# Kernel tuning notes

Hardware: AMD Instinct MI355X
Metric: run time of the kernel (lower is better)

The kernel has to match this reference:

```python
import jax, jax.numpy as jnp
import numpy as np

B, N, D = 4, 8192, 512
L, W, S = 64, 64, 32  # num_tokens, win_size, stride


def setup_inputs() -> dict:
    key = jax.random.key(0)
    ks = jax.random.split(key, 12)
    inp = {
        "feats": jax.random.normal(ks[0], (B, N, D), jnp.float32),
        "coords": jax.random.normal(ks[1], (B, N, 2), jnp.float32) * 100.0,
        "mask": jnp.zeros((B, N), dtype=bool),
        "z": jax.random.normal(ks[2], (L, D), jnp.float32) * 0.02,
        "Wq": jax.random.normal(ks[3], (D, D), jnp.float32) * 0.01,
        "Wk": jax.random.normal(ks[4], (D, D), jnp.float32) * 0.01,
        "Wv": jax.random.normal(ks[5], (D, D), jnp.float32) * 0.01,
        "W1": jax.random.normal(ks[6], (D, 2), jnp.float32) * 0.05,
        "b1": jnp.zeros((D,), jnp.float32),
        "W2": jax.random.normal(ks[7], (D, D), jnp.float32) * 0.01,
        "b2": jnp.zeros((D,), jnp.float32),
        "Wo": jax.random.normal(ks[8], (D, D), jnp.float32) * 0.01,
        "bo": jnp.zeros((D,), jnp.float32),
    }
    return inp


def reference(feats, coords, mask, z, Wq, Wk, Wv, W1, b1, W2, b2, Wo, bo):
    # mask is all-False: every token valid, N_valid == N, segments are
    # contiguous blocks of P = N // L tokens (seg_id = floor(i*L/N)).
    Bz, Nn, Dd = feats.shape
    Ll = z.shape[0]
    P = Nn // Ll  # tokens per segment

    # LayerNorm over feature dim (no affine, eps=1e-5 as in F.layer_norm)
    mu = feats.mean(-1, keepdims=True)
    var = feats.var(-1, keepdims=True)
    f_ln = (feats - mu) * jax.lax.rsqrt(var + 1e-5)

    # per-sample coordinate normalization (torch std is unbiased, ddof=1)
    c_mu = coords.mean(1, keepdims=True)
    c_sd = coords.std(1, keepdims=True, ddof=1) + 1e-8
    c_n = (coords - c_mu) / c_sd

    f_seg = f_ln.reshape(Bz, Ll, P, Dd)
    c_seg = c_n.reshape(Bz, Ll, P, 2)

    # static sliding windows within each segment (last window may be partial)
    starts = np.arange(0, P, S)                      # [nw]
    idx = starts[:, None] + np.arange(W)[None, :]    # [nw, W]
    valid = jnp.asarray(idx < P)                     # [nw, W] bool
    idx_c = np.minimum(idx, P - 1)
    cnt = valid.sum(-1).astype(feats.dtype)          # [nw]

    f_win = f_seg[:, :, idx_c]                       # [B,L,nw,W,D]
    c_win = c_seg[:, :, idx_c]                       # [B,L,nw,W,2]

    vmask = valid.astype(feats.dtype)[None, None, :, :, None]
    c_mean = (c_win * vmask).sum(3) / cnt[None, None, :, None]   # [B,L,nw,2]
    pos_in = c_win - c_mean[:, :, :, None, :]
    h = jax.nn.relu(jnp.einsum('blnwc,dc->blnwd', pos_in, W1) + b1)
    pos_bias = jnp.einsum('blnwd,ed->blnwe', h, W2) + b2

    q = z @ Wq.T                                     # [L,D]
    k = jnp.einsum('blnwd,ed->blnwe', f_win, Wk) + pos_bias
    v = jnp.einsum('blnwd,ed->blnwe', f_win, Wv)

    temperature = jnp.sqrt(jnp.asarray(Dd, feats.dtype))
    logits = jnp.einsum('ld,blnwd->blnw', q, k) / temperature
    logits = jnp.clip(logits, -10.0, 10.0)
    logits = jnp.where(valid[None, None], logits, -jnp.inf)
    attn = jax.nn.softmax(logits, axis=-1)           # [B,L,nw,W]

    z_win = jnp.einsum('blnw,blnwd->blnd', attn, v)  # [B,L,nw,D]
    z_l = z_win.mean(2)                              # average over windows
    return z_l @ Wo.T + bo                           # [B,L,D]
```

## Files before the change

### kernel.cpp

```cpp
#include <hip/hip_runtime.h>

#define Bz 4
#define Nn 8192
#define Dd 512
#define Ll 64
#define Pp 128
#define Ww 64
#define Ss 32
#define NW 4

__global__ __launch_bounds__(256) void pre1(
    const float* __restrict__ coords, const float* __restrict__ b2,
    const float* __restrict__ Wq, const float* __restrict__ Wk,
    const float* __restrict__ W2,
    const float* __restrict__ Wv, const float* __restrict__ Wo,
    float* __restrict__ cstats,
    float* __restrict__ M1, float* __restrict__ M2,
    float* __restrict__ WvoT, float* __restrict__ vb8) {
    __shared__ float As[64][68];
    __shared__ float Bs[64][68];
    __shared__ float b2s[64];
    __shared__ double dred[16];
    int bid = blockIdx.x, tid = threadIdx.x;
    int wv = tid >> 6, lane = tid & 63;

    if (bid < 192) {
        int role = bid >> 6;
        int wb = bid & 63;
        int m0 = (wb >> 3) * 64;
        int n0 = (wb & 7) * 64;
        const float* Amat = (role == 2) ? Wv : Wq;
        const float* Bmat = (role == 0) ? Wk : (role == 1) ? W2 : Wo;
        float* Cmat = (role == 0) ? M1 : (role == 1) ? M2 : WvoT;
        int tx = tid & 15, ty = tid >> 4;
        float4 acc[4];
#pragma unroll
        for (int i = 0; i < 4; ++i) acc[i] = make_float4(0.f, 0.f, 0.f, 0.f);

        for (int k0 = 0; k0 < Dd; k0 += 64) {
            {
                int kk = tid >> 4, q4 = (tid & 15) * 4;
#pragma unroll
                for (int i = 0; i < 4; ++i) {
                    int k = kk + 16 * i;
                    *(float4*)&As[k][q4] =
                        *(const float4*)&Amat[(size_t)(k0 + k) * Dd + m0 + q4];
                }
                if (role != 2) {
#pragma unroll
                    for (int i = 0; i < 4; ++i) {
                        int k = kk + 16 * i;
                        *(float4*)&Bs[k][q4] =
                            *(const float4*)&Bmat[(size_t)(k0 + k) * Dd + n0 + q4];
                    }
                } else {
                    int d = tid >> 2;
#pragma unroll
                    for (int j = 0; j < 4; ++j) {
                        int c0 = (tid & 3) * 16 + 4 * j;
                        float4 v = *(const float4*)&Bmat[(size_t)(n0 + d) * Dd + k0 + c0];
                        Bs[c0 + 0][d] = v.x; Bs[c0 + 1][d] = v.y;
                        Bs[c0 + 2][d] = v.z; Bs[c0 + 3][d] = v.w;
                    }
                }
            }
            __syncthreads();
#pragma unroll 8
            for (int kk = 0; kk < 64; ++kk) {
                float4 a4 = *(const float4*)&As[kk][ty * 4];
                float4 b4 = *(const float4*)&Bs[kk][tx * 4];
                acc[0].x = fmaf(a4.x, b4.x, acc[0].x); acc[0].y = fmaf(a4.x, b4.y, acc[0].y);
                acc[0].z = fmaf(a4.x, b4.z, acc[0].z); acc[0].w = fmaf(a4.x, b4.w, acc[0].w);
                acc[1].x = fmaf(a4.y, b4.x, acc[1].x); acc[1].y = fmaf(a4.y, b4.y, acc[1].y);
                acc[1].z = fmaf(a4.y, b4.z, acc[1].z); acc[1].w = fmaf(a4.y, b4.w, acc[1].w);
                acc[2].x = fmaf(a4.z, b4.x, acc[2].x); acc[2].y = fmaf(a4.z, b4.y, acc[2].y);
                acc[2].z = fmaf(a4.z, b4.z, acc[2].z); acc[2].w = fmaf(a4.z, b4.w, acc[2].w);
                acc[3].x = fmaf(a4.w, b4.x, acc[3].x); acc[3].y = fmaf(a4.w, b4.y, acc[3].y);
                acc[3].z = fmaf(a4.w, b4.z, acc[3].z); acc[3].w = fmaf(a4.w, b4.w, acc[3].w);
            }
            __syncthreads();
        }
#pragma unroll
        for (int i = 0; i < 4; ++i)
            *(float4*)&Cmat[(size_t)(m0 + ty * 4 + i) * Dd + n0 + tx * 4] = acc[i];
    } else if (bid < 200) {
        int j = bid - 192;
        if (tid < 64) b2s[tid] = b2[j * 64 + tid];
        __syncthreads();
        float a0 = 0.f, a1 = 0.f;
#pragma unroll 4
        for (int ee = 0; ee < 64; ++ee) {
            int e = j * 64 + ee;
            float be = b2s[ee];
            a0 = fmaf(be, Wq[(size_t)e * Dd + tid], a0);
            a1 = fmaf(be, Wq[(size_t)e * Dd + tid + 256], a1);
        }
        vb8[j * Dd + tid] = a0;
        vb8[j * Dd + tid + 256] = a1;
    } else {
        int b = bid - 200;
        double sx = 0, sy = 0, sxx = 0, syy = 0;
        const float4* cp = (const float4*)(coords + (size_t)b * Nn * 2);
        for (int i = tid; i < Nn / 2; i += 256) {
            float4 v = cp[i];
            sx  += (double)v.x + (double)v.z;
            sy  += (double)v.y + (double)v.w;
            sxx += (double)v.x * v.x + (double)v.z * v.z;
            syy += (double)v.y * v.y + (double)v.w * v.w;
        }
        for (int o = 32; o > 0; o >>= 1) {
            sx  += __shfl_down(sx,  o); sy  += __shfl_down(sy,  o);
            sxx += __shfl_down(sxx, o); syy += __shfl_down(syy, o);
        }
        if (lane == 0) {
            dred[wv * 4 + 0] = sx;  dred[wv * 4 + 1] = sy;
            dred[wv * 4 + 2] = sxx; dred[wv * 4 + 3] = syy;
        }
        __syncthreads();
        if (tid == 0) {
            double tx = 0, ty = 0, txx = 0, tyy = 0;
            for (int i = 0; i < 4; ++i) {
                tx += dred[i * 4 + 0]; ty += dred[i * 4 + 1];
                txx += dred[i * 4 + 2]; tyy += dred[i * 4 + 3];
            }
            const double N = (double)Nn;
            double mux = tx / N, muy = ty / N;
            double vx = (txx - N * mux * mux) / (N - 1.0);
            double vy = (tyy - N * muy * muy) / (N - 1.0);
            cstats[b * 4 + 0] = (float)mux;
            cstats[b * 4 + 1] = (float)muy;
            cstats[b * 4 + 2] = (float)sqrt(vx) + 1e-8f;
            cstats[b * 4 + 3] = (float)sqrt(vy) + 1e-8f;
        }
    }
}

__global__ __launch_bounds__(256) void qkg_k(
    const float* __restrict__ z, const float* __restrict__ M1,
    const float* __restrict__ M2, const float* __restrict__ vb8,
    float* __restrict__ QK, float* __restrict__ G,
    float* __restrict__ sqk4, float* __restrict__ qb2) {
    __shared__ float zs[Dd];
    __shared__ float pq[8][128];
    __shared__ float pg[8][128];
    __shared__ float red[8];
    int bid = blockIdx.x, tid = threadIdx.x;
    int l = bid & 63, ch = bid >> 6;
    int wv = tid >> 6, lane = tid & 63;

    zs[tid]       = z[(size_t)l * Dd + tid];
    zs[tid + 256] = z[(size_t)l * Dd + tid + 256];
    __syncthreads();

    if (ch == 0) {
        float vba = 0.f, vbb = 0.f;
#pragma unroll
        for (int j = 0; j < 8; ++j) {
            vba += vb8[j * Dd + tid];
            vbb += vb8[j * Dd + tid + 256];
        }
        float p = zs[tid] * vba + zs[tid + 256] * vbb;
        for (int o = 32; o > 0; o >>= 1) p += __shfl_xor(p, o);
        if (lane == 0) red[4 + wv] = p;
    }

    {
        int qd = tid & 31, h = tid >> 5;
        int cb = ch * 128 + qd * 4;
        float4 aq = make_float4(0.f, 0.f, 0.f, 0.f);
        float4 ag = make_float4(0.f, 0.f, 0.f, 0.f);
        for (int d = h * 64; d < h * 64 + 64; ++d) {
            float zd = zs[d];
            float4 m1 = *(const float4*)&M1[(size_t)d * Dd + cb];
            float4 m2 = *(const float4*)&M2[(size_t)d * Dd + cb];
            aq.x = fmaf(zd, m1.x, aq.x); aq.y = fmaf(zd, m1.y, aq.y);
            aq.z = fmaf(zd, m1.z, aq.z); aq.w = fmaf(zd, m1.w, aq.w);
            ag.x = fmaf(zd, m2.x, ag.x); ag.y = fmaf(zd, m2.y, ag.y);
            ag.z = fmaf(zd, m2.z, ag.z); ag.w = fmaf(zd, m2.w, ag.w);
        }
        *(float4*)&pq[h][qd * 4] = aq;
        *(float4*)&pg[h][qd * 4] = ag;
    }
    __syncthreads();
    if (tid < 128) {
        float vq = 0.f, vg = 0.f;
#pragma unroll
        for (int hh = 0; hh < 8; ++hh) { vq += pq[hh][tid]; vg += pg[hh][tid]; }
        QK[(size_t)l * Dd + ch * 128 + tid] = vq;
        G [(size_t)l * Dd + ch * 128 + tid] = vg;
        float s = vq;
        for (int o = 32; o > 0; o >>= 1) s += __shfl_xor(s, o);
        if (lane == 0) red[wv] = s;
    }
    __syncthreads();
    if (tid == 0) sqk4[ch * 64 + l] = red[0] + red[1];
    if (ch == 0 && tid == 32) qb2[l] = red[4] + red[5] + red[6] + red[7];
}

__global__ __launch_bounds__(1024) void attn2(
    const float* __restrict__ feats, const float* __restrict__ coords,
    const float* __restrict__ cstats,
    const float* __restrict__ QKm, const float* __restrict__ Gm,
    const float* __restrict__ sqk4, const float* __restrict__ qb2,
    const float* __restrict__ W1, const float* __restrict__ b1,
    const float* __restrict__ WvoT, const float* __restrict__ bo,
    float* __restrict__ out) {
    __shared__ float  qk_s[Dd];
    __shared__ float4 wpack[Dd];
    __shared__ float  scx[Pp], scy[Pp];
    __shared__ float  smu[Pp], srs[Pp], sa[Pp];
    __shared__ float  shs[NW * Ww];
    __shared__ float  sar[NW][Ww];
    __shared__ float  swt[Pp];
    __shared__ float  scm[8];
    __shared__ float  s2red[NW];
    __shared__ float  soff;
    __shared__ float  red8[8][Dd];

    int bx = blockIdx.x;
    int l = bx & 63, b = bx >> 6;
    int tid = threadIdx.x;
    int wv = tid >> 6, lane = tid & 63;

    const float* fbase = feats + (size_t)bx * Pp * Dd;
    int rb = wv * 8;
    float4 A0[4], A1[4], B0[4], B1[4];
#pragma unroll
    for (int i = 0; i < 4; ++i) {
        const float4* fr = (const float4*)(fbase + (size_t)(rb + i) * Dd);
        A0[i] = fr[lane * 2]; A1[i] = fr[lane * 2 + 1];
    }
#pragma unroll
    for (int i = 0; i < 4; ++i) {
        const float4* fr = (const float4*)(fbase + (size_t)(rb + 4 + i) * Dd);
        B0[i] = fr[lane * 2]; B1[i] = fr[lane * 2 + 1];
    }

    if (tid < Dd) {
        qk_s[tid] = QKm[l * Dd + tid];
    } else {
        int t = tid - Dd;
        wpack[t] = make_float4(W1[2 * t], W1[2 * t + 1], b1[t], Gm[l * Dd + t]);
    }
    if (tid < Pp) {
        int row = bx * Pp + tid;
        float x = coords[(size_t)row * 2], y = coords[(size_t)row * 2 + 1];
        scx[tid] = (x - cstats[b * 4 + 0]) / cstats[b * 4 + 2];
        scy[tid] = (y - cstats[b * 4 + 1]) / cstats[b * 4 + 3];
    }
    float sqk_l = sqk4[l] + sqk4[64 + l] + sqk4[128 + l] + sqk4[192 + l];
    float qb2_l = qb2[l];
    __syncthreads();

    if (wv < 4) {
        int n = wv, w = lane;
        int nv = (n == 3) ? 32 : 64;
        float cx = (w < nv) ? scx[n * Ss + w] : 0.f;
        float cy = (w < nv) ? scy[n * Ss + w] : 0.f;
        for (int o = 32; o > 0; o >>= 1) { cx += __shfl_xor(cx, o); cy += __shfl_xor(cy, o); }
        if (lane == 0) { scm[n] = cx / (float)nv; scm[4 + n] = cy / (float)nv; }
    }

    float4 q0 = ((const float4*)qk_s)[lane * 2];
    float4 q1 = ((const float4*)qk_s)[lane * 2 + 1];
    {
        float sP[4], ssP[4], aP[4];
#pragma unroll
        for (int i = 0; i < 4; ++i) {
            float4 v0 = A0[i], v1 = A1[i];
            sP[i]  = v0.x + v0.y + v0.z + v0.w + v1.x + v1.y + v1.z + v1.w;
            ssP[i] = v0.x * v0.x + v0.y * v0.y + v0.z * v0.z + v0.w * v0.w
                   + v1.x * v1.x + v1.y * v1.y + v1.z * v1.z + v1.w * v1.w;
            aP[i]  = v0.x * q0.x + v0.y * q0.y + v0.z * q0.z + v0.w * q0.w
                   + v1.x * q1.x + v1.y * q1.y + v1.z * q1.z + v1.w * q1.w;
        }
#pragma unroll
        for (int o = 32; o > 0; o >>= 1) {
#pragma unroll
            for (int i = 0; i < 4; ++i) {
                sP[i] += __shfl_xor(sP[i], o); ssP[i] += __shfl_xor(ssP[i], o);
                aP[i] += __shfl_xor(aP[i], o);
            }
        }
        if (lane == 0) {
#pragma unroll
            for (int i = 0; i < 4; ++i) {
                int r = rb + i;
                float mu  = sP[i] * (1.f / (float)Dd);
                float var = ssP[i] * (1.f / (float)Dd) - mu * mu;
                smu[r] = mu; srs[r] = 1.f / sqrtf(var + 1e-5f); sa[r] = aP[i];
            }
        }
#pragma unroll
        for (int i = 0; i < 4; ++i) {
            float4 v0 = B0[i], v1 = B1[i];
            sP[i]  = v0.x + v0.y + v0.z + v0.w + v1.x + v1.y + v1.z + v1.w;
            ssP[i] = v0.x * v0.x + v0.y * v0.y + v0.z * v0.z + v0.w * v0.w
                   + v1.x * v1.x + v1.y * v1.y + v1.z * v1.z + v1.w * v1.w;
            aP[i]  = v0.x * q0.x + v0.y * q0.y + v0.z * q0.z + v0.w * q0.w
                   + v1.x * q1.x + v1.y * q1.y + v1.z * q1.z + v1.w * q1.w;
        }
#pragma unroll
        for (int o = 32; o > 0; o >>= 1) {
#pragma unroll
            for (int i = 0; i < 4; ++i) {
                sP[i] += __shfl_xor(sP[i], o); ssP[i] += __shfl_xor(ssP[i], o);
                aP[i] += __shfl_xor(aP[i], o);
            }
        }
        if (lane == 0) {
#pragma unroll
            for (int i = 0; i < 4; ++i) {
                int r = rb + 4 + i;
                float mu  = sP[i] * (1.f / (float)Dd);
                float var = ssP[i] * (1.f / (float)Dd) - mu * mu;
                smu[r] = mu; srs[r] = 1.f / sqrtf(var + 1e-5f); sa[r] = aP[i];
            }
        }
    }
    __syncthreads();

    {
        int s = tid >> 2, q = tid & 3;
        int n = s >> 6, w = s & 63;
        int nv = (n == 3) ? 32 : 64;
        float hs = 0.f;
        if (w < nv) {
            int p = n * Ss + w;
            float px = scx[p] - scm[n], py = scy[p] - scm[4 + n];
            int d0 = q * 128;
#pragma unroll 4
            for (int d = d0; d < d0 + 128; ++d) {
                float4 c = wpack[d];
                hs = fmaf(c.w, fmaxf(fmaf(c.x, px, fmaf(c.y, py, c.z)), 0.f), hs);
            }
        }
        hs += __shfl_xor(hs, 1);
        hs += __shfl_xor(hs, 2);
        if (q == 0) shs[s] = hs;
    }
    __syncthreads();

    const float invtemp = 0.04419417382415922f;
    if (wv < 4) {
        int n = wv, w = lane;
        int nv = (n == 3) ? 32 : 64;
        int p = n * Ss + ((w < nv) ? w : 0);
        float lg = -1e30f;
        if (w < nv) {
            lg = (srs[p] * (sa[p] - smu[p] * sqk_l) + shs[n * Ww + w] + qb2_l) * invtemp;
            lg = fminf(fmaxf(lg, -10.f), 10.f);
        }
        float m = lg;
        for (int o = 32; o > 0; o >>= 1) m = fmaxf(m, __shfl_xor(m, o));
        float e = (w < nv) ? expf(lg - m) : 0.f;
        float ssum = e;
        for (int o = 32; o > 0; o >>= 1) ssum += __shfl_xor(ssum, o);
        float ar = (w < nv) ? (e / ssum) * srs[p] : 0.f;
        sar[n][w] = ar;
        float t2 = (w < nv) ? ar * smu[p] : 0.f;
        for (int o = 32; o > 0; o >>= 1) t2 += __shfl_xor(t2, o);
        if (lane == 0) s2red[n] = t2;
    }
    __syncthreads();

    if (tid < Pp) {
        int p = tid;
        int na = (p >> 5) - 1, nb = (p >> 5);
        float wt = 0.f;
        if (na >= 0 && na <= 3) wt += sar[na][p - na * Ss];
        if (nb <= 3)            wt += sar[nb][p - nb * Ss];
        swt[p] = wt;
    }
    if (tid == 0) soff = 0.25f * (s2red[0] + s2red[1] + s2red[2] + s2red[3]);
    __syncthreads();

    {
        int g = tid >> 7, c4 = tid & 127;
        const float4* f4 = (const float4*)fbase;
        float4 acc = make_float4(0.f, 0.f, 0.f, 0.f);
#pragma unroll 4
        for (int p = g; p < Pp; p += 8) {
            float wt = swt[p];
            float4 v = f4[p * 128 + c4];
            acc.x = fmaf(wt, v.x, acc.x);
            acc.y = fmaf(wt, v.y, acc.y);
            acc.z = fmaf(wt, v.z, acc.z);
            acc.w = fmaf(wt, v.w, acc.w);
        }
        *(float4*)&red8[g][c4 * 4] = acc;
    }
    __syncthreads();
    if (tid < Dd) {
        float v = 0.f;
#pragma unroll
        for (int w = 0; w < 8; ++w) v += red8[w][tid];
        qk_s[tid] = 0.25f * v - soff;
    }
    __syncthreads();

    {
        int h = tid >> 7, cq = (tid & 127) * 4;
        float4 acc = make_float4(0.f, 0.f, 0.f, 0.f);
#pragma unroll 4
        for (int e = h * 64; e < h * 64 + 64; ++e) {
            float fe = qk_s[e];
            float4 w = *(const float4*)&WvoT[(size_t)e * Dd + cq];
            acc.x = fmaf(fe, w.x, acc.x);
            acc.y = fmaf(fe, w.y, acc.y);
            acc.z = fmaf(fe, w.z, acc.z);
            acc.w = fmaf(fe, w.w, acc.w);
        }
        *(float4*)&red8[h][cq] = acc;
    }
    __syncthreads();
    if (tid < Dd) {
        out[(size_t)bx * Dd + tid] = bo[tid]
            + red8[0][tid] + red8[1][tid] + red8[2][tid] + red8[3][tid]
            + red8[4][tid] + red8[5][tid] + red8[6][tid] + red8[7][tid];
    }
}

extern "C" void kernel_launch(void* const* d_in, const int* in_sizes, int n_in,
                              void* d_out, int out_size, void* d_ws, size_t ws_size,
                              hipStream_t stream) {
    const float* feats  = (const float*)d_in[0];
    const float* coords = (const float*)d_in[1];
    const float* z  = (const float*)d_in[3];
    const float* Wq = (const float*)d_in[4];
    const float* Wk = (const float*)d_in[5];
    const float* Wv = (const float*)d_in[6];
    const float* W1 = (const float*)d_in[7];
    const float* b1 = (const float*)d_in[8];
    const float* W2 = (const float*)d_in[9];
    const float* b2 = (const float*)d_in[10];
    const float* Wo = (const float*)d_in[11];
    const float* bo = (const float*)d_in[12];
    float* out = (float*)d_out;

    float* ws = (float*)d_ws;
    float* cstats = ws;
    float* M1     = ws + 16;
    float* M2     = M1 + Dd * Dd;
    float* WvoT   = M2 + Dd * Dd;
    float* vb8    = WvoT + Dd * Dd;
    float* QK     = vb8 + 8 * Dd;
    float* G      = QK + Ll * Dd;
    float* sqk4   = G + Ll * Dd;
    float* qb2    = sqk4 + 256;

    pre1<<<204, 256, 0, stream>>>(coords, b2, Wq, Wk, W2, Wv, Wo,
                                  cstats, M1, M2, WvoT, vb8);
    qkg_k<<<256, 256, 0, stream>>>(z, M1, M2, vb8, QK, G, sqk4, qb2);
    attn2<<<Bz * Ll, 1024, 0, stream>>>(feats, coords, cstats,
                                        QK, G, sqk4, qb2, W1, b1,
                                        WvoT, bo, out);
}
```

Baseline: 187.1 us.

## Keep feats rows in registers and reuse them for the weighted-sum pass

The attn2 kernel now loads each wave's 8 feature rows into registers once, using a lane/lane+64 float4 layout, after the first barrier. Those registers feed both the LayerNorm/q-dot statistics and the later weighted sum, so the second global read of feats is gone. Window coordinate means are computed per wave in registers, which removes the scm shared array and one barrier, and the position MLP now runs before the stats pass to help hide load latency. The cost is higher register pressure from 16 float4 values held per thread across several phases, plus a larger 16-row shared reduction buffer.

```diff
diff --git a/kernel.cpp b/kernel.cpp
--- a/kernel.cpp
+++ b/kernel.cpp
@@ -212,29 +212,14 @@
     __shared__ float  shs[NW * Ww];
     __shared__ float  sar[NW][Ww];
     __shared__ float  swt[Pp];
-    __shared__ float  scm[8];
     __shared__ float  s2red[NW];
     __shared__ float  soff;
-    __shared__ float  red8[8][Dd];
+    __shared__ float  red16[16][Dd];
 
     int bx = blockIdx.x;
     int l = bx & 63, b = bx >> 6;
     int tid = threadIdx.x;
     int wv = tid >> 6, lane = tid & 63;
-
-    const float* fbase = feats + (size_t)bx * Pp * Dd;
-    int rb = wv * 8;
-    float4 A0[4], A1[4], B0[4], B1[4];
-#pragma unroll
-    for (int i = 0; i < 4; ++i) {
-        const float4* fr = (const float4*)(fbase + (size_t)(rb + i) * Dd);
-        A0[i] = fr[lane * 2]; A1[i] = fr[lane * 2 + 1];
-    }
-#pragma unroll
-    for (int i = 0; i < 4; ++i) {
-        const float4* fr = (const float4*)(fbase + (size_t)(rb + 4 + i) * Dd);
-        B0[i] = fr[lane * 2]; B1[i] = fr[lane * 2 + 1];
-    }
 
     if (tid < Dd) {
         qk_s[tid] = QKm[l * Dd + tid];
@@ -252,73 +237,26 @@
     float qb2_l = qb2[l];
     __syncthreads();
 
-    if (wv < 4) {
-        int n = wv, w = lane;
+    const float* fbase = feats + (size_t)bx * Pp * Dd;
+    int rb = wv * 8;
+    float4 f0[8], f1[8];
+#pragma unroll
+    for (int i = 0; i < 8; ++i) {
+        const float4* fr = (const float4*)(fbase + (size_t)(rb + i) * Dd);
+        f0[i] = fr[lane];
+        f1[i] = fr[lane + 64];
+    }
+    __builtin_amdgcn_sched_barrier(0);
+
+    float cmx[4], cmy[4];
+#pragma unroll
+    for (int n = 0; n < 4; ++n) {
         int nv = (n == 3) ? 32 : 64;
-        float cx = (w < nv) ? scx[n * Ss + w] : 0.f;
-        float cy = (w < nv) ? scy[n * Ss + w] : 0.f;
+        float cx = (lane < nv) ? scx[n * Ss + lane] : 0.f;
+        float cy = (lane < nv) ? scy[n * Ss + lane] : 0.f;
         for (int o = 32; o > 0; o >>= 1) { cx += __shfl_xor(cx, o); cy += __shfl_xor(cy, o); }
-        if (lane == 0) { scm[n] = cx / (float)nv; scm[4 + n] = cy / (float)nv; }
-    }
-
-    float4 q0 = ((const float4*)qk_s)[lane * 2];
-    float4 q1 = ((const float4*)qk_s)[lane * 2 + 1];
-    {
-        float sP[4], ssP[4], aP[4];
-#pragma unroll
-        for (int i = 0; i < 4; ++i) {
-            float4 v0 = A0[i], v1 = A1[i];
-            sP[i]  = v0.x + v0.y + v0.z + v0.w + v1.x + v1.y + v1.z + v1.w;
-            ssP[i] = v0.x * v0.x + v0.y * v0.y + v0.z * v0.z + v0.w * v0.w
-                   + v1.x * v1.x + v1.y * v1.y + v1.z * v1.z + v1.w * v1.w;
-            aP[i]  = v0.x * q0.x + v0.y * q0.y + v0.z * q0.z + v0.w * q0.w
-                   + v1.x * q1.x + v1.y * q1.y + v1.z * q1.z + v1.w * q1.w;
-        }
-#pragma unroll
-        for (int o = 32; o > 0; o >>= 1) {
-#pragma unroll
-            for (int i = 0; i < 4; ++i) {
-                sP[i] += __shfl_xor(sP[i], o); ssP[i] += __shfl_xor(ssP[i], o);
-                aP[i] += __shfl_xor(aP[i], o);
-            }
-        }
-        if (lane == 0) {
-#pragma unroll
-            for (int i = 0; i < 4; ++i) {
-                int r = rb + i;
-                float mu  = sP[i] * (1.f / (float)Dd);
-                float var = ssP[i] * (1.f / (float)Dd) - mu * mu;
-                smu[r] = mu; srs[r] = 1.f / sqrtf(var + 1e-5f); sa[r] = aP[i];
-            }
-        }
-#pragma unroll
-        for (int i = 0; i < 4; ++i) {
-            float4 v0 = B0[i], v1 = B1[i];
-            sP[i]  = v0.x + v0.y + v0.z + v0.w + v1.x + v1.y + v1.z + v1.w;
-            ssP[i] = v0.x * v0.x + v0.y * v0.y + v0.z * v0.z + v0.w * v0.w
-                   + v1.x * v1.x + v1.y * v1.y + v1.z * v1.z + v1.w * v1.w;
-            aP[i]  = v0.x * q0.x + v0.y * q0.y + v0.z * q0.z + v0.w * q0.w
-                   + v1.x * q1.x + v1.y * q1.y + v1.z * q1.z + v1.w * q1.w;
-        }
-#pragma unroll
-        for (int o = 32; o > 0; o >>= 1) {
-#pragma unroll
-            for (int i = 0; i < 4; ++i) {
-                sP[i] += __shfl_xor(sP[i], o); ssP[i] += __shfl_xor(ssP[i], o);
-                aP[i] += __shfl_xor(aP[i], o);
-            }
-        }
-        if (lane == 0) {
-#pragma unroll
-            for (int i = 0; i < 4; ++i) {
-                int r = rb + 4 + i;
-                float mu  = sP[i] * (1.f / (float)Dd);
-                float var = ssP[i] * (1.f / (float)Dd) - mu * mu;
-                smu[r] = mu; srs[r] = 1.f / sqrtf(var + 1e-5f); sa[r] = aP[i];
-            }
-        }
-    }
-    __syncthreads();
+        cmx[n] = cx / (float)nv; cmy[n] = cy / (float)nv;
+    }
 
     {
         int s = tid >> 2, q = tid & 3;
@@ -327,7 +265,7 @@
         float hs = 0.f;
         if (w < nv) {
             int p = n * Ss + w;
-            float px = scx[p] - scm[n], py = scy[p] - scm[4 + n];
+            float px = scx[p] - cmx[n], py = scy[p] - cmy[n];
             int d0 = q * 128;
 #pragma unroll 4
             for (int d = d0; d < d0 + 128; ++d) {
@@ -338,6 +276,41 @@
         hs += __shfl_xor(hs, 1);
         hs += __shfl_xor(hs, 2);
         if (q == 0) shs[s] = hs;
+    }
+
+    {
+        float4 q0 = ((const float4*)qk_s)[lane];
+        float4 q1 = ((const float4*)qk_s)[lane + 64];
+#pragma unroll
+        for (int b2i = 0; b2i < 8; b2i += 4) {
+            float sP[4], ssP[4], aP[4];
+#pragma unroll
+            for (int i = 0; i < 4; ++i) {
+                float4 v0 = f0[b2i + i], v1 = f1[b2i + i];
+                sP[i]  = v0.x + v0.y + v0.z + v0.w + v1.x + v1.y + v1.z + v1.w;
+                ssP[i] = v0.x * v0.x + v0.y * v0.y + v0.z * v0.z + v0.w * v0.w
+                       + v1.x * v1.x + v1.y * v1.y + v1.z * v1.z + v1.w * v1.w;
+                aP[i]  = v0.x * q0.x + v0.y * q0.y + v0.z * q0.z + v0.w * q0.w
+                       + v1.x * q1.x + v1.y * q1.y + v1.z * q1.z + v1.w * q1.w;
+            }
+#pragma unroll
+            for (int o = 32; o > 0; o >>= 1) {
+#pragma unroll
+                for (int i = 0; i < 4; ++i) {
+                    sP[i] += __shfl_xor(sP[i], o); ssP[i] += __shfl_xor(ssP[i], o);
+                    aP[i] += __shfl_xor(aP[i], o);
+                }
+            }
+            if (lane == 0) {
+#pragma unroll
+                for (int i = 0; i < 4; ++i) {
+                    int r = rb + b2i + i;
+                    float mu  = sP[i] * (1.f / (float)Dd);
+                    float var = ssP[i] * (1.f / (float)Dd) - mu * mu;
+                    smu[r] = mu; srs[r] = 1.f / sqrtf(var + 1e-5f); sa[r] = aP[i];
+                }
+            }
+        }
     }
     __syncthreads();
 
@@ -376,25 +349,24 @@
     __syncthreads();
 
     {
-        int g = tid >> 7, c4 = tid & 127;
-        const float4* f4 = (const float4*)fbase;
-        float4 acc = make_float4(0.f, 0.f, 0.f, 0.f);
-#pragma unroll 4
-        for (int p = g; p < Pp; p += 8) {
-            float wt = swt[p];
-            float4 v = f4[p * 128 + c4];
-            acc.x = fmaf(wt, v.x, acc.x);
-            acc.y = fmaf(wt, v.y, acc.y);
-            acc.z = fmaf(wt, v.z, acc.z);
-            acc.w = fmaf(wt, v.w, acc.w);
-        }
-        *(float4*)&red8[g][c4 * 4] = acc;
+        float4 a0 = make_float4(0.f, 0.f, 0.f, 0.f);
+        float4 a1 = make_float4(0.f, 0.f, 0.f, 0.f);
+#pragma unroll
+        for (int i = 0; i < 8; ++i) {
+            float wt = swt[rb + i];
+            a0.x = fmaf(wt, f0[i].x, a0.x); a0.y = fmaf(wt, f0[i].y, a0.y);
+            a0.z = fmaf(wt, f0[i].z, a0.z); a0.w = fmaf(wt, f0[i].w, a0.w);
+            a1.x = fmaf(wt, f1[i].x, a1.x); a1.y = fmaf(wt, f1[i].y, a1.y);
+            a1.z = fmaf(wt, f1[i].z, a1.z); a1.w = fmaf(wt, f1[i].w, a1.w);
+        }
+        *(float4*)&red16[wv][lane * 4]       = a0;
+        *(float4*)&red16[wv][256 + lane * 4] = a1;
     }
     __syncthreads();
     if (tid < Dd) {
         float v = 0.f;
 #pragma unroll
-        for (int w = 0; w < 8; ++w) v += red8[w][tid];
+        for (int w = 0; w < 16; ++w) v += red16[w][tid];
         qk_s[tid] = 0.25f * v - soff;
     }
     __syncthreads();
@@ -411,13 +383,13 @@
             acc.z = fmaf(fe, w.z, acc.z);
             acc.w = fmaf(fe, w.w, acc.w);
         }
-        *(float4*)&red8[h][cq] = acc;
+        *(float4*)&red16[h][cq] = acc;
     }
     __syncthreads();
     if (tid < Dd) {
         out[(size_t)bx * Dd + tid] = bo[tid]
-            + red8[0][tid] + red8[1][tid] + red8[2][tid] + red8[3][tid]
-            + red8[4][tid] + red8[5][tid] + red8[6][tid] + red8[7][tid];
+            + red16[0][tid] + red16[1][tid] + red16[2][tid] + red16[3][tid]
+            + red16[4][tid] + red16[5][tid] + red16[6][tid] + red16[7][tid];
     }
 }
 
```

Result: faster. 174.6 us (-6.7%).
